# Kernel optimization log

Measured on AMD Instinct MI355X. Metric: run time of the kernel, lower is better.

## Reference

```python
import jax, jax.numpy as jnp
import numpy as np

N_POINTS = 64
N_COLS = 500000
N_ANGS = N_POINTS * (N_POINTS - 1) // 2  # 2016


def setup_inputs() -> dict:
    key = jax.random.key(0)
    k1, k2 = jax.random.split(key)
    X = jax.random.normal(k1, (N_POINTS, N_COLS), dtype=jnp.float32)
    angles = 0.1 * jax.random.normal(k2, (N_ANGS,), dtype=jnp.float32)
    mus = jnp.ones((N_POINTS,), dtype=jnp.float32)
    return {"X": X, "angles": angles, "mus": mus}


def reference(X, angles, mus):
    # X: [n, m]; apply n(n-1)/2 sequential Givens rotations over row pairs
    # in order (iTop, iBtm) for iTop < iBtm, then scale rows by mus.
    # Original torch math per pair: vt' = c*vt - s*vb ; vb' = s*vt + c*vb.
    n = X.shape[0]
    top_np, btm_np = np.triu_indices(n, k=1)  # row-major order matches the double loop
    top = jnp.asarray(top_np, dtype=jnp.int32)
    btm = jnp.asarray(btm_np, dtype=jnp.int32)

    def step(Y, inp):
        a, it, ib = inp
        c = jnp.cos(a)
        s = jnp.sin(a)
        vt = Y[it]  # [m]
        vb = Y[ib]  # [m]
        Y = Y.at[it].set(c * vt - s * vb)
        Y = Y.at[ib].set(s * vt + c * vb)
        return Y, None

    Y, _ = jax.lax.scan(step, X, (angles, top, btm))
    return Y * mus[:, None]
```

## Files before the change

kernel.cpp:

```cpp
#include <hip/hip_runtime.h>

#define NPTS   64
#define NCOLS  500000
#define NANG   2016
#define NFULL  7812
#define TPB    1024
#define BLOCKS 512

typedef __attribute__((ext_vector_type(8))) short bf16x8;
typedef __attribute__((ext_vector_type(4))) float f32x4;

static __device__ __forceinline__ short f2bf(float f) {
    union { float f; unsigned u; } uf; uf.f = f;
    unsigned u = uf.u;
    unsigned r = (u + 0x7fffu + ((u >> 16) & 1u)) >> 16;
    return (short)r;
}

static __host__ __device__ constexpr int rotS(int i) { return 63 * i - i * (i - 1) / 2; }

__device__ __forceinline__ void chain_rolled(const float2* __restrict__ csn,
                                             float* __restrict__ P,
                                             int lane, int I0, int I1) {
    for (int r = 0; r < 64; ++r) P[r * 64 + lane] = (r == lane) ? 1.0f : 0.0f;
    int k = 0;
#pragma unroll 1
    for (int i = I0; i < I1; ++i) {
        float t = P[i * 64 + lane];
#pragma unroll 8
        for (int ib = i + 1; ib < 64; ++ib, ++k) {
            float2 cs = csn[k];
            float b = P[ib * 64 + lane];
            P[ib * 64 + lane] = cs.y * t + cs.x * b;
            t = cs.x * t - cs.y * b;
        }
        P[i * 64 + lane] = t;
    }
}

__global__ __launch_bounds__(TPB, 8) void fused_ortho(const float* __restrict__ X,
                                                      const float* __restrict__ angles,
                                                      const float* __restrict__ mus,
                                                      float* __restrict__ out) {
    __shared__ __align__(16) float sm[4032 + 3 * 4096];
    const int tid  = threadIdx.x;
    const int lane = tid & 63;
    const int wave = __builtin_amdgcn_readfirstlane(tid >> 6);

    float2* csn = (float2*)sm;
    for (int t = tid; t < NANG; t += TPB) {
        float s, c;
        sincosf(angles[t], &s, &c);
        csn[t] = make_float2(c, s);
    }
    __syncthreads();

    float* P0 = sm + 4032;
    float* P1 = sm + 8128;
    float* P2 = sm + 12224;

    if (wave == 0)      chain_rolled(csn,            P0, lane,  0, 12);
    else if (wave == 1) chain_rolled(csn + rotS(12), P1, lane, 12, 26);
    else if (wave == 2) chain_rolled(csn + rotS(26), P2, lane, 26, 63);
    __syncthreads();

    {
        const int row0 = wave * 4;
        float acc[4] = {0.f, 0.f, 0.f, 0.f};
#pragma unroll 4
        for (int k0 = 0; k0 < 64; k0 += 4) {
            float lo0 = P0[(k0 + 0) * 64 + lane];
            float lo1 = P0[(k0 + 1) * 64 + lane];
            float lo2 = P0[(k0 + 2) * 64 + lane];
            float lo3 = P0[(k0 + 3) * 64 + lane];
#pragma unroll
            for (int r = 0; r < 4; ++r) {
                const f32x4 h = *(const f32x4*)&P1[(row0 + r) * 64 + k0];
                acc[r] = fmaf(h[0], lo0, acc[r]);
                acc[r] = fmaf(h[1], lo1, acc[r]);
                acc[r] = fmaf(h[2], lo2, acc[r]);
                acc[r] = fmaf(h[3], lo3, acc[r]);
            }
        }
        __syncthreads();
#pragma unroll
        for (int r = 0; r < 4; ++r) P0[(row0 + r) * 64 + lane] = acc[r];
    }
    __syncthreads();

    {
        const int row0 = wave * 4;
        float acc[4] = {0.f, 0.f, 0.f, 0.f};
#pragma unroll 4
        for (int k0 = 0; k0 < 64; k0 += 4) {
            float lo0 = P0[(k0 + 0) * 64 + lane];
            float lo1 = P0[(k0 + 1) * 64 + lane];
            float lo2 = P0[(k0 + 2) * 64 + lane];
            float lo3 = P0[(k0 + 3) * 64 + lane];
#pragma unroll
            for (int r = 0; r < 4; ++r) {
                const f32x4 h = *(const f32x4*)&P2[(row0 + r) * 64 + k0];
                acc[r] = fmaf(h[0], lo0, acc[r]);
                acc[r] = fmaf(h[1], lo1, acc[r]);
                acc[r] = fmaf(h[2], lo2, acc[r]);
                acc[r] = fmaf(h[3], lo3, acc[r]);
            }
        }
#pragma unroll
        for (int r = 0; r < 4; ++r)
            P1[(row0 + r) * 64 + lane] = acc[r] * mus[row0 + r];
    }
    __syncthreads();

    const int laneN = lane & 15;
    const int quad  = lane >> 4;

    bf16x8 afrag[4][2];
#pragma unroll
    for (int t = 0; t < 4; ++t) {
#pragma unroll
        for (int q = 0; q < 2; ++q) {
            const float* src = P1 + (t * 16 + laneN) * 64 + q * 32 + quad * 8;
            bf16x8 f;
#pragma unroll
            for (int j = 0; j < 8; ++j) f[j] = f2bf(src[j]);
            afrag[t][q] = f;
        }
    }

    const int gw = blockIdx.x * 16 + wave;

    if (gw < NFULL) {
        const long col0 = (long)gw * 64 + 4 * laneN;
        const float* xb = X + col0;

        bf16x8 bfrag[4][2];
#pragma unroll
        for (int q = 0; q < 2; ++q) {
#pragma unroll
            for (int j = 0; j < 8; ++j) {
                const int kk = q * 32 + quad * 8 + j;
                f32x4 v = *(const f32x4*)(xb + (long)kk * NCOLS);
#pragma unroll
                for (int u = 0; u < 4; ++u)
                    bfrag[u][q][j] = f2bf(v[u]);
            }
        }

#pragma unroll
        for (int t = 0; t < 4; ++t) {
            f32x4 acc[4];
#pragma unroll
            for (int u = 0; u < 4; ++u) {
                f32x4 a = {0.f, 0.f, 0.f, 0.f};
                a = __builtin_amdgcn_mfma_f32_16x16x32_bf16(afrag[t][0], bfrag[u][0], a, 0, 0, 0);
                a = __builtin_amdgcn_mfma_f32_16x16x32_bf16(afrag[t][1], bfrag[u][1], a, 0, 0, 0);
                acc[u] = a;
            }
#pragma unroll
            for (int rr = 0; rr < 4; ++rr) {
                const int row = t * 16 + quad * 4 + rr;
                f32x4 o = { acc[0][rr], acc[1][rr], acc[2][rr], acc[3][rr] };
                __builtin_nontemporal_store(o, (f32x4*)(out + (long)row * NCOLS + col0));
            }
        }
    } else if (gw < NFULL + 2) {
        const int tw  = gw - NFULL;
        const int col = NFULL * 64 + tw * 16 + laneN;
        const float* xb = X + col;
        bf16x8 bfrag[2];
#pragma unroll
        for (int q = 0; q < 2; ++q) {
            bf16x8 f;
#pragma unroll
            for (int j = 0; j < 8; ++j)
                f[j] = f2bf(xb[(long)(q * 32 + quad * 8 + j) * NCOLS]);
            bfrag[q] = f;
        }
#pragma unroll
        for (int t = 0; t < 4; ++t) {
            f32x4 a = {0.f, 0.f, 0.f, 0.f};
            a = __builtin_amdgcn_mfma_f32_16x16x32_bf16(afrag[t][0], bfrag[0], a, 0, 0, 0);
            a = __builtin_amdgcn_mfma_f32_16x16x32_bf16(afrag[t][1], bfrag[1], a, 0, 0, 0);
#pragma unroll
            for (int rr = 0; rr < 4; ++rr)
                __builtin_nontemporal_store(a[rr],
                    out + (long)(t * 16 + quad * 4 + rr) * NCOLS + col);
        }
    }
}

extern "C" void kernel_launch(void* const* d_in, const int* in_sizes, int n_in,
                              void* d_out, int out_size, void* d_ws, size_t ws_size,
                              hipStream_t stream) {
    const float* X      = (const float*)d_in[0];
    const float* angles = (const float*)d_in[1];
    const float* mus    = (const float*)d_in[2];
    fused_ortho<<<BLOCKS, TPB, 0, stream>>>(X, angles, mus, (float*)d_out);
}
```

Measured before the change: 330.6 us.

## Halve block size, register-resident rotation chains, prefetch X during setup

Blocks shrink to 512 threads, and each wave now handles two 64-column tiles using a software-pipelined load/convert/MFMA sequence. The three Givens chains are rebalanced to 21 rows each and kept in a 64-entry register array with predicated rotations instead of LDS read-modify-write. Non-chain waves issue their X loads before the chain barrier so memory latency overlaps the rotation setup. The cost is heavier per-block setup amortized over twice the columns, higher register pressure, and fewer resident waves per CU.

```diff
diff --git a/kernel.cpp b/kernel.cpp
--- a/kernel.cpp
+++ b/kernel.cpp
@@ -4,8 +4,9 @@
 #define NCOLS  500000
 #define NANG   2016
 #define NFULL  7812
-#define TPB    1024
+#define TPB    512
 #define BLOCKS 512
+#define NWAVES (BLOCKS * 8)
 
 typedef __attribute__((ext_vector_type(8))) short bf16x8;
 typedef __attribute__((ext_vector_type(4))) float f32x4;
@@ -17,56 +18,114 @@
     return (short)r;
 }
 
-static __host__ __device__ constexpr int rotS(int i) { return 63 * i - i * (i - 1) / 2; }
-
-__device__ __forceinline__ void chain_rolled(const float2* __restrict__ csn,
-                                             float* __restrict__ P,
-                                             int lane, int I0, int I1) {
-    for (int r = 0; r < 64; ++r) P[r * 64 + lane] = (r == lane) ? 1.0f : 0.0f;
-    int k = 0;
+__device__ __forceinline__ void chunk_reg(const float2* __restrict__ csn,
+                                          float* __restrict__ P,
+                                          int lane, int I0, int I1) {
+    float q[64];
+#pragma unroll
+    for (int r = 0; r < 64; ++r) q[r] = (r == lane) ? 1.0f : 0.0f;
+
 #pragma unroll 1
     for (int i = I0; i < I1; ++i) {
-        float t = P[i * 64 + lane];
-#pragma unroll 8
-        for (int ib = i + 1; ib < 64; ++ib, ++k) {
-            float2 cs = csn[k];
-            float b = P[ib * 64 + lane];
-            P[ib * 64 + lane] = cs.y * t + cs.x * b;
-            t = cs.x * t - cs.y * b;
-        }
-        P[i * 64 + lane] = t;
-    }
-}
-
-__global__ __launch_bounds__(TPB, 8) void fused_ortho(const float* __restrict__ X,
+        float t = q[0];
+#pragma unroll
+        for (int j = 1; j < 64; ++j) t = (j == i) ? q[j] : t;
+
+        const int base = 63 * i - (i * (i - 1)) / 2 - i - 1;
+#pragma unroll
+        for (int j = 1; j < 64; ++j) {
+            const float2 cs = csn[base + j];
+            const bool  act = (j > i);
+            const float c = act ? cs.x : 1.0f;
+            const float s = act ? cs.y : 0.0f;
+            const float b = q[j];
+            q[j] = fmaf(s, t, c * b);
+            t    = fmaf(c, t, -(s * b));
+        }
+#pragma unroll
+        for (int j = 0; j < 64; ++j) q[j] = (j == i) ? t : q[j];
+    }
+
+#pragma unroll
+    for (int r = 0; r < 64; ++r) P[r * 64 + lane] = q[r];
+}
+
+__device__ __forceinline__ void issue8(const float* __restrict__ xb, int kbase,
+                                       f32x4 xq[8]) {
+#pragma unroll
+    for (int j = 0; j < 8; ++j)
+        xq[j] = *(const f32x4*)(xb + (long)(kbase + j) * NCOLS);
+}
+
+template<int Q>
+__device__ __forceinline__ void cvt8(const f32x4 xq[8], bf16x8 bfrag[4][2]) {
+#pragma unroll
+    for (int j = 0; j < 8; ++j)
+#pragma unroll
+        for (int u = 0; u < 4; ++u)
+            bfrag[u][Q][j] = f2bf(xq[j][u]);
+}
+
+__device__ __forceinline__ void mfma_store(const bf16x8 afrag[4][2],
+                                           const bf16x8 bfrag[4][2],
+                                           float* __restrict__ out, long col0,
+                                           int quad) {
+#pragma unroll
+    for (int t = 0; t < 4; ++t) {
+        f32x4 acc[4];
+#pragma unroll
+        for (int u = 0; u < 4; ++u) {
+            f32x4 a = {0.f, 0.f, 0.f, 0.f};
+            a = __builtin_amdgcn_mfma_f32_16x16x32_bf16(afrag[t][0], bfrag[u][0], a, 0, 0, 0);
+            a = __builtin_amdgcn_mfma_f32_16x16x32_bf16(afrag[t][1], bfrag[u][1], a, 0, 0, 0);
+            acc[u] = a;
+        }
+#pragma unroll
+        for (int rr = 0; rr < 4; ++rr) {
+            const int row = t * 16 + quad * 4 + rr;
+            f32x4 o = { acc[0][rr], acc[1][rr], acc[2][rr], acc[3][rr] };
+            __builtin_nontemporal_store(o, (f32x4*)(out + (long)row * NCOLS + col0));
+        }
+    }
+}
+
+__global__ __launch_bounds__(TPB, 4) void fused_ortho(const float* __restrict__ X,
                                                       const float* __restrict__ angles,
                                                       const float* __restrict__ mus,
                                                       float* __restrict__ out) {
     __shared__ __align__(16) float sm[4032 + 3 * 4096];
-    const int tid  = threadIdx.x;
-    const int lane = tid & 63;
-    const int wave = __builtin_amdgcn_readfirstlane(tid >> 6);
+    const int tid   = threadIdx.x;
+    const int lane  = tid & 63;
+    const int wave  = __builtin_amdgcn_readfirstlane(tid >> 6);
+    const int laneN = lane & 15;
+    const int quad  = lane >> 4;
 
     float2* csn = (float2*)sm;
-    for (int t = tid; t < NANG; t += TPB) {
-        float s, c;
-        sincosf(angles[t], &s, &c);
-        csn[t] = make_float2(c, s);
-    }
-    __syncthreads();
-
     float* P0 = sm + 4032;
     float* P1 = sm + 8128;
     float* P2 = sm + 12224;
 
-    if (wave == 0)      chain_rolled(csn,            P0, lane,  0, 12);
-    else if (wave == 1) chain_rolled(csn + rotS(12), P1, lane, 12, 26);
-    else if (wave == 2) chain_rolled(csn + rotS(26), P2, lane, 26, 63);
-    __syncthreads();
+    const int  gw   = blockIdx.x * 8 + wave;
+    const long col0 = (long)gw * 64 + 4 * laneN;
+    f32x4 xq[8];
+
+    for (int a = tid; a < NANG; a += TPB) {
+        float s, c;
+        sincosf(angles[a], &s, &c);
+        csn[a] = make_float2(c, s);
+    }
+    __syncthreads();
+
+    if (wave == 0)      chunk_reg(csn, P0, lane,  0, 21);
+    else if (wave == 1) chunk_reg(csn, P1, lane, 21, 42);
+    else if (wave == 2) chunk_reg(csn, P2, lane, 42, 63);
+    else                issue8(X + col0, quad * 8, xq);
+    __syncthreads();
+    if (wave < 3) issue8(X + col0, quad * 8, xq);
 
     {
-        const int row0 = wave * 4;
-        float acc[4] = {0.f, 0.f, 0.f, 0.f};
+        const int row0 = wave * 8;
+        float acc[8] = {0.f, 0.f, 0.f, 0.f, 0.f, 0.f, 0.f, 0.f};
 #pragma unroll 4
         for (int k0 = 0; k0 < 64; k0 += 4) {
             float lo0 = P0[(k0 + 0) * 64 + lane];
@@ -74,7 +133,7 @@
             float lo2 = P0[(k0 + 2) * 64 + lane];
             float lo3 = P0[(k0 + 3) * 64 + lane];
 #pragma unroll
-            for (int r = 0; r < 4; ++r) {
+            for (int r = 0; r < 8; ++r) {
                 const f32x4 h = *(const f32x4*)&P1[(row0 + r) * 64 + k0];
                 acc[r] = fmaf(h[0], lo0, acc[r]);
                 acc[r] = fmaf(h[1], lo1, acc[r]);
@@ -84,13 +143,13 @@
         }
         __syncthreads();
 #pragma unroll
-        for (int r = 0; r < 4; ++r) P0[(row0 + r) * 64 + lane] = acc[r];
+        for (int r = 0; r < 8; ++r) P0[(row0 + r) * 64 + lane] = acc[r];
     }
     __syncthreads();
 
     {
-        const int row0 = wave * 4;
-        float acc[4] = {0.f, 0.f, 0.f, 0.f};
+        const int row0 = wave * 8;
+        float acc[8] = {0.f, 0.f, 0.f, 0.f, 0.f, 0.f, 0.f, 0.f};
 #pragma unroll 4
         for (int k0 = 0; k0 < 64; k0 += 4) {
             float lo0 = P0[(k0 + 0) * 64 + lane];
@@ -98,7 +157,7 @@
             float lo2 = P0[(k0 + 2) * 64 + lane];
             float lo3 = P0[(k0 + 3) * 64 + lane];
 #pragma unroll
-            for (int r = 0; r < 4; ++r) {
+            for (int r = 0; r < 8; ++r) {
                 const f32x4 h = *(const f32x4*)&P2[(row0 + r) * 64 + k0];
                 acc[r] = fmaf(h[0], lo0, acc[r]);
                 acc[r] = fmaf(h[1], lo1, acc[r]);
@@ -107,13 +166,10 @@
             }
         }
 #pragma unroll
-        for (int r = 0; r < 4; ++r)
+        for (int r = 0; r < 8; ++r)
             P1[(row0 + r) * 64 + lane] = acc[r] * mus[row0 + r];
     }
     __syncthreads();
-
-    const int laneN = lane & 15;
-    const int quad  = lane >> 4;
 
     bf16x8 afrag[4][2];
 #pragma unroll
@@ -128,60 +184,42 @@
         }
     }
 
-    const int gw = blockIdx.x * 16 + wave;
-
-    if (gw < NFULL) {
-        const long col0 = (long)gw * 64 + 4 * laneN;
-        const float* xb = X + col0;
-
-        bf16x8 bfrag[4][2];
-#pragma unroll
-        for (int q = 0; q < 2; ++q) {
-#pragma unroll
-            for (int j = 0; j < 8; ++j) {
-                const int kk = q * 32 + quad * 8 + j;
-                f32x4 v = *(const f32x4*)(xb + (long)kk * NCOLS);
-#pragma unroll
-                for (int u = 0; u < 4; ++u)
-                    bfrag[u][q][j] = f2bf(v[u]);
-            }
-        }
-
-#pragma unroll
-        for (int t = 0; t < 4; ++t) {
-            f32x4 acc[4];
-#pragma unroll
-            for (int u = 0; u < 4; ++u) {
-                f32x4 a = {0.f, 0.f, 0.f, 0.f};
-                a = __builtin_amdgcn_mfma_f32_16x16x32_bf16(afrag[t][0], bfrag[u][0], a, 0, 0, 0);
-                a = __builtin_amdgcn_mfma_f32_16x16x32_bf16(afrag[t][1], bfrag[u][1], a, 0, 0, 0);
-                acc[u] = a;
-            }
-#pragma unroll
-            for (int rr = 0; rr < 4; ++rr) {
-                const int row = t * 16 + quad * 4 + rr;
-                f32x4 o = { acc[0][rr], acc[1][rr], acc[2][rr], acc[3][rr] };
-                __builtin_nontemporal_store(o, (f32x4*)(out + (long)row * NCOLS + col0));
-            }
-        }
-    } else if (gw < NFULL + 2) {
-        const int tw  = gw - NFULL;
+    const long s1   = (long)gw + NWAVES;
+    const bool has1 = (s1 < NFULL);
+    const long col1 = s1 * 64 + 4 * laneN;
+
+    bf16x8 bfrag[4][2];
+    cvt8<0>(xq, bfrag);
+    issue8(X + col0, 32 + quad * 8, xq);
+    cvt8<1>(xq, bfrag);
+    if (has1) issue8(X + col1, quad * 8, xq);
+    mfma_store(afrag, bfrag, out, col0, quad);
+
+    if (has1) {
+        cvt8<0>(xq, bfrag);
+        issue8(X + col1, 32 + quad * 8, xq);
+        cvt8<1>(xq, bfrag);
+        mfma_store(afrag, bfrag, out, col1, quad);
+    }
+
+    if (gw >= NWAVES - 2) {
+        const int tw  = gw - (NWAVES - 2);
         const int col = NFULL * 64 + tw * 16 + laneN;
         const float* xb = X + col;
-        bf16x8 bfrag[2];
+        bf16x8 bt[2];
 #pragma unroll
         for (int q = 0; q < 2; ++q) {
             bf16x8 f;
 #pragma unroll
             for (int j = 0; j < 8; ++j)
                 f[j] = f2bf(xb[(long)(q * 32 + quad * 8 + j) * NCOLS]);
-            bfrag[q] = f;
+            bt[q] = f;
         }
 #pragma unroll
         for (int t = 0; t < 4; ++t) {
             f32x4 a = {0.f, 0.f, 0.f, 0.f};
-            a = __builtin_amdgcn_mfma_f32_16x16x32_bf16(afrag[t][0], bfrag[0], a, 0, 0, 0);
-            a = __builtin_amdgcn_mfma_f32_16x16x32_bf16(afrag[t][1], bfrag[1], a, 0, 0, 0);
+            a = __builtin_amdgcn_mfma_f32_16x16x32_bf16(afrag[t][0], bt[0], a, 0, 0, 0);
+            a = __builtin_amdgcn_mfma_f32_16x16x32_bf16(afrag[t][1], bt[1], a, 0, 0, 0);
 #pragma unroll
             for (int rr = 0; rr < 4; ++rr)
                 __builtin_nontemporal_store(a[rr],
```

New measurement: 282.4 us. -14.6%, faster.
